# Optimization experiments

Hardware: AMD Instinct MI355X
Metric: run time of the kernel (lower is better)

The kernel has to match this reference:

```python
import jax, jax.numpy as jnp
import numpy as np

D = 32
B = 4096
T = 256
HIDDEN = 64
DT = 0.005


def setup_inputs() -> dict:
    key = jax.random.key(0)
    ks = jax.random.split(key, 6)
    s1 = 1.0 / np.sqrt(D + 1)
    s2 = 1.0 / np.sqrt(HIDDEN)
    return {
        "z0": jax.random.normal(ks[0], (B, D), dtype=jnp.float32),
        "ts": jnp.arange(T, dtype=jnp.float32) * DT,
        "noise": jax.random.normal(ks[1], (T - 1, B, D), dtype=jnp.float32),
        "W1": jax.random.normal(ks[2], (D + 1, HIDDEN), dtype=jnp.float32) * s1,
        "b1": jnp.zeros((HIDDEN,), dtype=jnp.float32),
        "W2": jax.random.normal(ks[3], (HIDDEN, HIDDEN), dtype=jnp.float32) * s2,
        "b2": jnp.zeros((HIDDEN,), dtype=jnp.float32),
        "W3": jax.random.normal(ks[4], (HIDDEN, D), dtype=jnp.float32) * s2,
        "b3": jnp.zeros((D,), dtype=jnp.float32),
        "log_std": jnp.full((D,), -1.0, dtype=jnp.float32),
    }


def reference(z0, ts, noise, W1, b1, W2, b2, W3, b3, log_std):
    """Euler-Maruyama integration of the posterior SDE.

    dz = f_phi(t, z) dt + diag(exp(log_std)) dW,  dW = sqrt(dt) * noise.
    Returns ys of shape [T, B, D] with ys[0] = z0 (matches torchsde.sdeint).
    """
    std = jnp.exp(log_std)  # [D], constant diagonal diffusion
    dts = ts[1:] - ts[:-1]  # [T-1]

    def drift(t, y):
        # MLP on cat([t, y]): Linear -> tanh -> Linear -> tanh -> Linear
        tt = jnp.broadcast_to(t, (y.shape[0], 1)).astype(y.dtype)
        h = jnp.tanh(jnp.concatenate([tt, y], axis=-1) @ W1 + b1)
        h = jnp.tanh(h @ W2 + b2)
        return h @ W3 + b3  # [B, D]

    def step(y, xs):
        t, dt, dw = xs
        y_next = y + drift(t, y) * dt + std * jnp.sqrt(dt) * dw
        return y_next, y_next

    _, ys = jax.lax.scan(step, z0, (ts[:-1], dts, noise))
    return jnp.concatenate([z0[None], ys], axis=0)  # [T, B, D]
```

## Files before the change

### kernel.cpp

```cpp
#include <hip/hip_runtime.h>

#define NB 4096
#define NT 256

typedef __bf16 bf16x8 __attribute__((ext_vector_type(8)));
typedef __bf16 bf16x4 __attribute__((ext_vector_type(4)));
typedef float f32x4 __attribute__((ext_vector_type(4)));
typedef unsigned int u32;
typedef unsigned int u32x4 __attribute__((ext_vector_type(4)));
typedef unsigned long long u64;

static __device__ __forceinline__ f32x4 mfma16(bf16x8 a, bf16x8 b, f32x4 c) {
  return __builtin_amdgcn_mfma_f32_16x16x32_bf16(a, b, c, 0, 0, 0);
}

static __device__ __forceinline__ float ftanh(float x) {
  float a = x * 2.885390082f;
  a = fminf(fmaxf(a, -64.0f), 64.0f);
  float e = __builtin_amdgcn_exp2f(a);
  float r = __builtin_amdgcn_rcpf(e + 1.0f);
  return __builtin_fmaf(-2.0f, r, 1.0f);
}

static __device__ __forceinline__ u64 pack4(const f32x4& v) {
  bf16x4 p;
  p[0] = (__bf16)ftanh(v[0]);
  p[1] = (__bf16)ftanh(v[1]);
  p[2] = (__bf16)ftanh(v[2]);
  p[3] = (__bf16)ftanh(v[3]);
  return __builtin_bit_cast(u64, p);
}

static __device__ __forceinline__ bf16x8 frag2(u64 lo, u64 hi) {
  u32x4 v;
  v[0] = (u32)lo; v[1] = (u32)(lo >> 32);
  v[2] = (u32)hi; v[3] = (u32)(hi >> 32);
  return __builtin_bit_cast(bf16x8, v);
}

__global__ __launch_bounds__(256) void sde_kernel(
    const float* __restrict__ z0, const float* __restrict__ ts,
    const float* __restrict__ noise, const float* __restrict__ W1,
    const float* __restrict__ b1, const float* __restrict__ W2,
    const float* __restrict__ b2, const float* __restrict__ W3,
    const float* __restrict__ b3, const float* __restrict__ log_std,
    float* __restrict__ out) {
  (void)ts;
  __shared__ u64 h1x[4][64];
  __shared__ u64 h2x[4][64];

  const int lane = threadIdx.x & 63;
  const int wv = threadIdx.x >> 6;
  const int c = lane & 15;
  const int g = lane >> 4;
  const int R = blockIdx.x * 16 + c;

  bf16x8 a1;
  bf16x8 a2[2];
  bf16x8 a3[2][2];
#pragma unroll
  for (int j = 0; j < 8; ++j) {
    int k = 16 * (j >> 2) + 4 * g + (j & 3);
    a1[j] = (__bf16)W1[(1 + k) * 64 + 16 * wv + c];
  }
#pragma unroll
  for (int kf = 0; kf < 2; ++kf)
#pragma unroll
    for (int j = 0; j < 8; ++j) {
      int k = 32 * kf + 16 * (j >> 2) + 4 * g + (j & 3);
      a2[kf][j] = (__bf16)W2[k * 64 + 16 * wv + c];
    }
#pragma unroll
  for (int ot = 0; ot < 2; ++ot)
#pragma unroll
    for (int kf = 0; kf < 2; ++kf)
#pragma unroll
      for (int j = 0; j < 8; ++j) {
        int k = 32 * kf + 16 * (j >> 2) + 4 * g + (j & 3);
        a3[ot][kf][j] = (__bf16)W3[k * 32 + 16 * ot + c];
      }

  f32x4 b1v, w1r0, b2v;
#pragma unroll
  for (int r = 0; r < 4; ++r) {
    int d = 16 * wv + 4 * g + r;
    b1v[r] = b1[d];
    w1r0[r] = W1[d];
    b2v[r] = b2[d];
  }
  f32x4 b3v[2], stdv[2];
#pragma unroll
  for (int ot = 0; ot < 2; ++ot)
#pragma unroll
    for (int r = 0; r < 4; ++r) {
      int d = 16 * ot + 4 * g + r;
      b3v[ot][r] = b3[d];
      stdv[ot][r] = expf(log_std[d]);
    }

  f32x4 y0v = *reinterpret_cast<const f32x4*>(z0 + (size_t)R * 32 + 4 * g);
  f32x4 y1v = *reinterpret_cast<const f32x4*>(z0 + (size_t)R * 32 + 16 + 4 * g);
  if (wv == 0)
    *reinterpret_cast<f32x4*>(out + (size_t)R * 32 + 4 * g) = y0v;
  if (wv == 1)
    *reinterpret_cast<f32x4*>(out + (size_t)R * 32 + 16 + 4 * g) = y1v;

  bf16x8 yb;
#pragma unroll
  for (int j = 0; j < 8; ++j)
    yb[j] = (__bf16)((j >> 2) ? y1v[j & 3] : y0v[j & 3]);

  const float* nzp0 = noise + ((size_t)0 * NB + R) * 32 + 4 * g;
  f32x4 nz0 = *reinterpret_cast<const f32x4*>(nzp0);
  f32x4 nz1 = *reinterpret_cast<const f32x4*>(nzp0 + 16);

  for (int t = 0; t < NT - 1; ++t) {
    int tn = (t < NT - 2) ? (t + 1) : (NT - 2);
    const float* nzp = noise + ((size_t)tn * NB + R) * 32 + 4 * g;
    f32x4 nzn0 = *reinterpret_cast<const f32x4*>(nzp);
    f32x4 nzn1 = *reinterpret_cast<const f32x4*>(nzp + 16);

    float tcur = (float)t * 0.005f;
    float dtv = (float)(t + 1) * 0.005f - tcur;
    float sdt = sqrtf(dtv);

    f32x4 cinit = b1v + tcur * w1r0;
    f32x4 d1 = mfma16(a1, yb, cinit);
    h1x[wv][lane] = pack4(d1);
    __syncthreads();

    u64 q0 = h1x[0][lane], q1 = h1x[1][lane];
    u64 q2 = h1x[2][lane], q3 = h1x[3][lane];
    bf16x8 hb0 = frag2(q0, q1);
    bf16x8 hb1 = frag2(q2, q3);
    f32x4 d2 = mfma16(a2[1], hb1, mfma16(a2[0], hb0, b2v));
    h2x[wv][lane] = pack4(d2);
    __syncthreads();

    u64 p0 = h2x[0][lane], p1 = h2x[1][lane];
    u64 p2 = h2x[2][lane], p3 = h2x[3][lane];
    bf16x8 gb0 = frag2(p0, p1);
    bf16x8 gb1 = frag2(p2, p3);
    f32x4 d30 = mfma16(a3[0][1], gb1, mfma16(a3[0][0], gb0, b3v[0]));
    f32x4 d31 = mfma16(a3[1][1], gb1, mfma16(a3[1][0], gb0, b3v[1]));

    y0v = y0v + d30 * dtv + (stdv[0] * sdt) * nz0;
    y1v = y1v + d31 * dtv + (stdv[1] * sdt) * nz1;

    float* op = out + ((size_t)(t + 1) * NB + R) * 32 + 4 * g;
    if (wv == 0) *reinterpret_cast<f32x4*>(op) = y0v;
    if (wv == 1) *reinterpret_cast<f32x4*>(op + 16) = y1v;

#pragma unroll
    for (int j = 0; j < 8; ++j)
      yb[j] = (__bf16)((j >> 2) ? y1v[j & 3] : y0v[j & 3]);

    nz0 = nzn0;
    nz1 = nzn1;
  }
}

extern "C" void kernel_launch(void* const* d_in, const int* in_sizes, int n_in,
                              void* d_out, int out_size, void* d_ws, size_t ws_size,
                              hipStream_t stream) {
  (void)in_sizes; (void)n_in; (void)out_size; (void)d_ws; (void)ws_size;
  const float* z0   = (const float*)d_in[0];
  const float* ts   = (const float*)d_in[1];
  const float* nz   = (const float*)d_in[2];
  const float* W1   = (const float*)d_in[3];
  const float* b1   = (const float*)d_in[4];
  const float* W2   = (const float*)d_in[5];
  const float* b2   = (const float*)d_in[6];
  const float* W3   = (const float*)d_in[7];
  const float* b3   = (const float*)d_in[8];
  const float* lstd = (const float*)d_in[9];
  float* out = (float*)d_out;
  hipLaunchKernelGGL(sde_kernel, dim3(NB / 16), dim3(256), 0, stream,
                     z0, ts, nz, W1, b1, W2, b2, W3, b3, lstd, out);
}
```

Before: 192.4 us.

## Compute full second layer per wave to remove one barrier per step

Each wave now computes all four 16-column output tiles of the second MLP layer redundantly, so the second shared-memory exchange and its __syncthreads are removed. The first-layer exchange buffer is double-buffered by step parity, so the remaining single barrier per step stays safe. The tanh clamp is also dropped. In exchange each wave issues four times the layer-2 MFMAs and tanh evaluations and holds more weight registers, and unclamped exp2 relies on inf/0 handling for large inputs.

```diff
diff --git a/kernel.cpp b/kernel.cpp
--- a/kernel.cpp
+++ b/kernel.cpp
@@ -15,11 +15,8 @@
 }
 
 static __device__ __forceinline__ float ftanh(float x) {
-  float a = x * 2.885390082f;
-  a = fminf(fmaxf(a, -64.0f), 64.0f);
-  float e = __builtin_amdgcn_exp2f(a);
-  float r = __builtin_amdgcn_rcpf(e + 1.0f);
-  return __builtin_fmaf(-2.0f, r, 1.0f);
+  float e = __builtin_amdgcn_exp2f(x * 2.885390082f);
+  return __builtin_fmaf(-2.0f, __builtin_amdgcn_rcpf(e + 1.0f), 1.0f);
 }
 
 static __device__ __forceinline__ u64 pack4(const f32x4& v) {
@@ -46,8 +43,7 @@
     const float* __restrict__ b3, const float* __restrict__ log_std,
     float* __restrict__ out) {
   (void)ts;
-  __shared__ u64 h1x[4][64];
-  __shared__ u64 h2x[4][64];
+  __shared__ u64 h1x[2][4][64];
 
   const int lane = threadIdx.x & 63;
   const int wv = threadIdx.x >> 6;
@@ -56,7 +52,7 @@
   const int R = blockIdx.x * 16 + c;
 
   bf16x8 a1;
-  bf16x8 a2[2];
+  bf16x8 a2[4][2];
   bf16x8 a3[2][2];
 #pragma unroll
   for (int j = 0; j < 8; ++j) {
@@ -64,12 +60,14 @@
     a1[j] = (__bf16)W1[(1 + k) * 64 + 16 * wv + c];
   }
 #pragma unroll
-  for (int kf = 0; kf < 2; ++kf)
+  for (int ot = 0; ot < 4; ++ot)
 #pragma unroll
-    for (int j = 0; j < 8; ++j) {
-      int k = 32 * kf + 16 * (j >> 2) + 4 * g + (j & 3);
-      a2[kf][j] = (__bf16)W2[k * 64 + 16 * wv + c];
-    }
+    for (int kf = 0; kf < 2; ++kf)
+#pragma unroll
+      for (int j = 0; j < 8; ++j) {
+        int k = 32 * kf + 16 * (j >> 2) + 4 * g + (j & 3);
+        a2[ot][kf][j] = (__bf16)W2[k * 64 + 16 * ot + c];
+      }
 #pragma unroll
   for (int ot = 0; ot < 2; ++ot)
 #pragma unroll
@@ -80,14 +78,18 @@
         a3[ot][kf][j] = (__bf16)W3[k * 32 + 16 * ot + c];
       }
 
-  f32x4 b1v, w1r0, b2v;
+  f32x4 b1v, w1r0;
 #pragma unroll
   for (int r = 0; r < 4; ++r) {
     int d = 16 * wv + 4 * g + r;
     b1v[r] = b1[d];
     w1r0[r] = W1[d];
-    b2v[r] = b2[d];
   }
+  f32x4 b2v[4];
+#pragma unroll
+  for (int ot = 0; ot < 4; ++ot)
+#pragma unroll
+    for (int r = 0; r < 4; ++r) b2v[ot][r] = b2[16 * ot + 4 * g + r];
   f32x4 b3v[2], stdv[2];
 #pragma unroll
   for (int ot = 0; ot < 2; ++ot)
@@ -124,23 +126,27 @@
     float dtv = (float)(t + 1) * 0.005f - tcur;
     float sdt = sqrtf(dtv);
 
-    f32x4 cinit = b1v + tcur * w1r0;
-    f32x4 d1 = mfma16(a1, yb, cinit);
-    h1x[wv][lane] = pack4(d1);
+    f32x4 d1 = mfma16(a1, yb, b1v + tcur * w1r0);
+    h1x[t & 1][wv][lane] = pack4(d1);
     __syncthreads();
 
-    u64 q0 = h1x[0][lane], q1 = h1x[1][lane];
-    u64 q2 = h1x[2][lane], q3 = h1x[3][lane];
+    u64 q0 = h1x[t & 1][0][lane], q1 = h1x[t & 1][1][lane];
+    u64 q2 = h1x[t & 1][2][lane], q3 = h1x[t & 1][3][lane];
     bf16x8 hb0 = frag2(q0, q1);
     bf16x8 hb1 = frag2(q2, q3);
-    f32x4 d2 = mfma16(a2[1], hb1, mfma16(a2[0], hb0, b2v));
-    h2x[wv][lane] = pack4(d2);
-    __syncthreads();
 
-    u64 p0 = h2x[0][lane], p1 = h2x[1][lane];
-    u64 p2 = h2x[2][lane], p3 = h2x[3][lane];
-    bf16x8 gb0 = frag2(p0, p1);
-    bf16x8 gb1 = frag2(p2, p3);
+    f32x4 d2[4];
+#pragma unroll
+    for (int ot = 0; ot < 4; ++ot)
+      d2[ot] = mfma16(a2[ot][1], hb1, mfma16(a2[ot][0], hb0, b2v[ot]));
+
+    bf16x8 gb0, gb1;
+#pragma unroll
+    for (int j = 0; j < 8; ++j) {
+      gb0[j] = (__bf16)ftanh(d2[(j >> 2)][j & 3]);
+      gb1[j] = (__bf16)ftanh(d2[2 + (j >> 2)][j & 3]);
+    }
+
     f32x4 d30 = mfma16(a3[0][1], gb1, mfma16(a3[0][0], gb0, b3v[0]));
     f32x4 d31 = mfma16(a3[1][1], gb1, mfma16(a3[1][0], gb0, b3v[1]));
 
```

After: 209.7 us. +9.0%, slower.
